# Kernel optimization log

Hardware: AMD Instinct MI355X
Metric: run time of the kernel (lower is better)

Reference implementation:

```python
import jax, jax.numpy as jnp
import numpy as np

N = 65536      # total atoms
D = 1024       # hidden_size (encoder output dim)
H = 2048       # ffn_hidden_size
OUT = 1        # output_size
M = 4096       # number of molecules (segments)


def _lin(k, fi, fo):
    return jax.random.normal(k, (fi, fo), jnp.float32) * (1.0 / np.sqrt(fi))


def setup_inputs() -> dict:
    key = jax.random.key(0)
    ks = jax.random.split(key, 14)
    hidden = jax.random.normal(ks[0], (N, D), jnp.float32)
    segment_ids = jnp.sort(jax.random.randint(ks[1], (N,), 0, M)).astype(jnp.int64)
    inp = {
        "hidden": hidden,
        "ffn_W1": _lin(ks[2], D, H), "ffn_b1": jnp.zeros((H,), jnp.float32),
        "ffn_W2": _lin(ks[3], H, H), "ffn_b2": jnp.zeros((H,), jnp.float32),
        "ffn_W3": _lin(ks[4], H, OUT), "ffn_b3": jnp.zeros((OUT,), jnp.float32),
        "wr_W1": _lin(ks[5], D, H), "wr_b1": jnp.zeros((H,), jnp.float32),
        "wr_W2": _lin(ks[6], H, H), "wr_b2": jnp.zeros((H,), jnp.float32),
        "wr_W3": _lin(ks[7], H, OUT), "wr_b3": jnp.ones((OUT,), jnp.float32),  # bias=1 keeps segment weight sums away from 0
        "segment_ids": segment_ids,
    }
    return inp


def _ffn(x, W1, b1, W2, b2, W3, b3):
    # Dropout(p) is identity in eval; activation = ReLU
    h = jax.nn.relu(x @ W1 + b1)
    h = jax.nn.relu(h @ W2 + b2)
    return h @ W3 + b3


def reference(hidden, ffn_W1, ffn_b1, ffn_W2, ffn_b2, ffn_W3, ffn_b3,
              wr_W1, wr_b1, wr_W2, wr_b2, wr_W3, wr_b3, segment_ids):
    seg = segment_ids.astype(jnp.int32)
    output = _ffn(hidden, ffn_W1, ffn_b1, ffn_W2, ffn_b2, ffn_W3, ffn_b3)   # [N, OUT]
    weights = _ffn(hidden, wr_W1, wr_b1, wr_W2, wr_b2, wr_W3, wr_b3)        # [N, OUT]
    # per-molecule sums over ALL elements of the segment slice (matches .sum())
    out_sum = jax.ops.segment_sum(output.sum(-1), seg, num_segments=M)      # [M]
    w_sum = jax.ops.segment_sum(weights.sum(-1), seg, num_segments=M)       # [M]
    ratio = (out_sum / w_sum)[seg][:, None]                                 # [N, 1]
    return output - weights * ratio
```

## Files before the change

kernel.cpp:

```cpp
#include <hip/hip_runtime.h>
#include <hip/hip_bf16.h>

#define DEVINL __device__ __forceinline__

typedef __attribute__((ext_vector_type(8))) short s8v;
typedef __attribute__((ext_vector_type(4))) float f4v;

using bf16 = __hip_bfloat16;
typedef unsigned short u16;

DEVINL u16 f2bu(float f) {
  bf16 h = __float2bfloat16(f);
  return *reinterpret_cast<u16*>(&h);
}

DEVINL void gload16(const void* g, void* l) {
  __builtin_amdgcn_global_load_lds((const __attribute__((address_space(1))) void*)g,
                                   (__attribute__((address_space(3))) void*)l, 16, 0, 0);
}

#define BAR()    __builtin_amdgcn_s_barrier()
#define LGKM(n)  asm volatile("s_waitcnt lgkmcnt(" #n ")" ::: "memory")
#define VM(n)    asm volatile("s_waitcnt vmcnt(" #n ")" ::: "memory")

__global__ void k_f32_to_bf16(const float* __restrict__ x, u16* __restrict__ y, long n4) {
  long i = (long)blockIdx.x * blockDim.x + threadIdx.x;
  if (i >= n4) return;
  float4 v = ((const float4*)x)[i];
  ushort4 o;
  o.x = f2bu(v.x); o.y = f2bu(v.y); o.z = f2bu(v.z); o.w = f2bu(v.w);
  ((ushort4*)y)[i] = o;
}

__global__ void k_transpose_bf16(const float* __restrict__ W, u16* __restrict__ Wt,
                                 int rows, int cols) {
  __shared__ float tile[32][33];
  const int tx = threadIdx.x, ty = threadIdx.y;
  const int c0 = blockIdx.x * 32, r0 = blockIdx.y * 32;
  #pragma unroll
  for (int i = ty; i < 32; i += 8)
    tile[i][tx] = W[(long)(r0 + i) * cols + (c0 + tx)];
  __syncthreads();
  #pragma unroll
  for (int i = ty; i < 32; i += 8)
    Wt[(long)(c0 + i) * rows + (r0 + tx)] = f2bu(tile[tx][i]);
}

extern __shared__ char smem[];

template<int EPI>
__global__ __launch_bounds__(512, 2)
void k_gemm8(const u16* __restrict__ A, const u16* __restrict__ Bt,
             u16* __restrict__ C, const float* __restrict__ bias,
             const float* __restrict__ w3, float* __restrict__ oacc,
             int N, int K) {
  const int tid = threadIdx.x;
  const int w = tid >> 6, lane = tid & 63;
  const int id = blockIdx.x;
  const int cpx = gridDim.x >> 3;
  const int sw = (id & 7) * cpx + (id >> 3);
  const int bn = sw & 7, bm = sw >> 3;

  const int wm = (w >> 2) * 128, wn = (w & 3) * 64;
  const int nt = K >> 6;

  f4v acc[8][4];
  #pragma unroll
  for (int i = 0; i < 8; ++i)
    #pragma unroll
    for (int jj = 0; jj < 4; ++jj)
      #pragma unroll
      for (int r = 0; r < 4; ++r) acc[i][jj][r] = 0.f;

  const int rowl = tid >> 2;
  const int jsw = (tid & 3) ^ ((rowl >> 1) & 3);
  const u16* gA = A + (long)(bm * 256 + rowl) * K + jsw * 8;
  const u16* gB = Bt + (long)(bn * 256 + rowl) * K + jsw * 8;
  const long cstr = (long)128 * K;
  const uint wb = (uint)w * 1024u;

  const uint swz = ((uint)((lane >> 4) ^ ((lane >> 1) & 3))) * 16u;
  const uint aoff = (uint)(wm + (lane & 15)) * 64u + swz;
  const uint boff = (uint)(wn + (lane & 15)) * 64u + swz + 32768u;

#define STAGE_A(pp, ks, t) do { \
    const u16* g_ = gA + (long)(t) * 64 + (ks) * 32; \
    char* l_ = smem + (uint)(pp) * 65536u + (uint)(ks) * 16384u + wb; \
    gload16(g_, l_); gload16(g_ + cstr, l_ + 8192); } while (0)
#define STAGE_B(pp, ks, t) do { \
    const u16* g_ = gB + (long)(t) * 64 + (ks) * 32; \
    char* l_ = smem + (uint)(pp) * 65536u + 32768u + (uint)(ks) * 16384u + wb; \
    gload16(g_, l_); gload16(g_ + cstr, l_ + 8192); } while (0)

#define RD_A(dst, base, ksb) do { \
    _Pragma("unroll") \
    for (int mi_ = 0; mi_ < 8; ++mi_) \
      dst[mi_] = *(const s8v*)(smem + (base) + (ksb) + aoff + (uint)mi_ * 1024u); } while (0)
#define RD_B(dst, base, ksb, c0) do { \
    dst[0] = *(const s8v*)(smem + (base) + (ksb) + boff + (uint)(c0) * 1024u); \
    dst[1] = *(const s8v*)(smem + (base) + (ksb) + boff + (uint)((c0) + 1) * 1024u); } while (0)

#define MFMA8(A_, B_, c0i, c1i) do { \
    __builtin_amdgcn_s_setprio(1); \
    _Pragma("unroll") \
    for (int mi_ = 0; mi_ < 8; ++mi_) { \
      acc[mi_][c0i] = __builtin_amdgcn_mfma_f32_16x16x32_bf16(A_[mi_], B_[0], acc[mi_][c0i], 0, 0, 0); \
      acc[mi_][c1i] = __builtin_amdgcn_mfma_f32_16x16x32_bf16(A_[mi_], B_[1], acc[mi_][c1i], 0, 0, 0); \
    } \
    __builtin_amdgcn_s_setprio(0); } while (0)

  s8v a0[8], a1[8], b01[2], b23[2];

  STAGE_A(0, 0, 0); STAGE_B(0, 0, 0); STAGE_A(0, 1, 0); STAGE_B(0, 1, 0);
  if (nt > 1) { STAGE_A(1, 0, 1); STAGE_B(1, 0, 1); VM(8); }
  else        { VM(4); }
  BAR();
  RD_A(a0, 0u, 0u); RD_B(b01, 0u, 0u, 0);

  for (int t = 0; t < nt; ++t) {
    const int p = t & 1, q = p ^ 1;
    const uint pb = (uint)p * 65536u, qb = (uint)q * 65536u;
    RD_B(b23, pb, 0u, 2);
    if (t + 1 < nt) STAGE_A(q, 1, t + 1);
    BAR(); LGKM(2);
    MFMA8(a0, b01, 0, 1);
    if (t + 1 < nt) { VM(6); } else { VM(0); }
    BAR();
    RD_A(a1, pb, 16384u); RD_B(b01, pb, 16384u, 0);
    if (t + 1 < nt) STAGE_B(q, 1, t + 1);
    LGKM(10);
    MFMA8(a0, b23, 2, 3);
    RD_B(b23, pb, 16384u, 2);
    if (t + 2 < nt) STAGE_A(p, 0, t + 2);
    BAR(); LGKM(2);
    MFMA8(a1, b01, 0, 1);
    if (t + 2 < nt) {
      STAGE_B(p, 0, t + 2);
      VM(8); BAR();
      RD_A(a0, qb, 0u); RD_B(b01, qb, 0u, 0);
      LGKM(10);
    } else if (t + 1 < nt) {
      VM(4); BAR();
      RD_A(a0, qb, 0u); RD_B(b01, qb, 0u, 0);
      LGKM(10);
    } else {
      BAR(); LGKM(0);
    }
    MFMA8(a1, b23, 2, 3);
  }

  const int crow = bm * 256 + wm + ((lane >> 4) << 2);
  const int ccol = bn * 256 + wn + (lane & 15);
  if (EPI == 1) {
    #pragma unroll
    for (int jj = 0; jj < 4; ++jj) {
      const float bb = bias[ccol + jj * 16];
      #pragma unroll
      for (int mi = 0; mi < 8; ++mi)
        #pragma unroll
        for (int r = 0; r < 4; ++r) {
          float v = acc[mi][jj][r] + bb;
          v = v > 0.f ? v : 0.f;
          C[(long)(crow + mi * 16 + r) * N + ccol + jj * 16] = f2bu(v);
        }
    }
  } else {
    float bb[4], ww[4];
    #pragma unroll
    for (int jj = 0; jj < 4; ++jj) { bb[jj] = bias[ccol + jj * 16]; ww[jj] = w3[ccol + jj * 16]; }
    #pragma unroll
    for (int mi = 0; mi < 8; ++mi)
      #pragma unroll
      for (int r = 0; r < 4; ++r) {
        float s = 0.f;
        #pragma unroll
        for (int jj = 0; jj < 4; ++jj) {
          float v = acc[mi][jj][r] + bb[jj];
          v = v > 0.f ? v : 0.f;
          s += v * ww[jj];
        }
        s += __shfl_xor(s, 1, 64);
        s += __shfl_xor(s, 2, 64);
        s += __shfl_xor(s, 4, 64);
        s += __shfl_xor(s, 8, 64);
        if ((lane & 15) == 0) atomicAdd(&oacc[crow + mi * 16 + r], s);
      }
  }
#undef STAGE_A
#undef STAGE_B
#undef RD_A
#undef RD_B
#undef MFMA8
}

__global__ void k_detect(const int* __restrict__ seg, int n, int* __restrict__ flag) {
  if (blockIdx.x == 0 && threadIdx.x == 0) flag[0] = (seg[n - 1] == 0) ? 1 : 0;
}

__global__ void k_segsum(const float* __restrict__ oacc, const float* __restrict__ wacc,
                         const int* __restrict__ seg, const int* __restrict__ flag,
                         const float* __restrict__ ob3, const float* __restrict__ wb3,
                         float* __restrict__ osum, float* __restrict__ wsum, int n) {
  int i = blockIdx.x * blockDim.x + threadIdx.x;
  if (i >= n) return;
  int s = flag[0] ? seg[2 * i] : seg[i];
  atomicAdd(&osum[s], oacc[i] + ob3[0]);
  atomicAdd(&wsum[s], wacc[i] + wb3[0]);
}

__global__ void k_final(const float* __restrict__ oacc, const float* __restrict__ wacc,
                        const int* __restrict__ seg, const int* __restrict__ flag,
                        const float* __restrict__ ob3, const float* __restrict__ wb3,
                        const float* __restrict__ osum, const float* __restrict__ wsum,
                        float* __restrict__ out, int n) {
  int i = blockIdx.x * blockDim.x + threadIdx.x;
  if (i >= n) return;
  int s = flag[0] ? seg[2 * i] : seg[i];
  float o = oacc[i] + ob3[0];
  float ww = wacc[i] + wb3[0];
  out[i] = o - ww * (osum[s] / wsum[s]);
}

extern "C" void kernel_launch(void* const* d_in, const int* in_sizes, int n_in,
                              void* d_out, int out_size, void* d_ws, size_t ws_size,
                              hipStream_t stream) {
  constexpr int NA = 65536, D = 1024, H = 2048, M = 4096;
  const float* hidden = (const float*)d_in[0];
  const float* fW1 = (const float*)d_in[1];
  const float* fb1 = (const float*)d_in[2];
  const float* fW2 = (const float*)d_in[3];
  const float* fb2 = (const float*)d_in[4];
  const float* fW3 = (const float*)d_in[5];
  const float* fb3 = (const float*)d_in[6];
  const float* wW1 = (const float*)d_in[7];
  const float* wb1 = (const float*)d_in[8];
  const float* wW2 = (const float*)d_in[9];
  const float* wb2 = (const float*)d_in[10];
  const float* wW3 = (const float*)d_in[11];
  const float* wb3 = (const float*)d_in[12];
  const int* seg = (const int*)d_in[13];
  float* out = (float*)d_out;

  char* ws = (char*)d_ws;
  size_t off = 0;
  auto alloc = [&](size_t bytes) { char* p = ws + off; off += (bytes + 255) & ~(size_t)255; return p; };
  u16* hbf  = (u16*)alloc((size_t)NA * D * 2);
  u16* w1tf = (u16*)alloc((size_t)H * D * 2);
  u16* w1tw = (u16*)alloc((size_t)H * D * 2);
  u16* w2tf = (u16*)alloc((size_t)H * H * 2);
  u16* w2tw = (u16*)alloc((size_t)H * H * 2);
  u16* h1   = (u16*)alloc((size_t)NA * H * 2);
  float* oacc = (float*)alloc((size_t)NA * 4);
  float* wacc = (float*)alloc((size_t)NA * 4);
  float* osum = (float*)alloc((size_t)M * 4);
  float* wsum = (float*)alloc((size_t)M * 4);
  int* flag = (int*)alloc(256);

  hipFuncSetAttribute((const void*)k_gemm8<1>, hipFuncAttributeMaxDynamicSharedMemorySize, 131072);
  hipFuncSetAttribute((const void*)k_gemm8<2>, hipFuncAttributeMaxDynamicSharedMemorySize, 131072);

  k_f32_to_bf16<<<(int)((long)NA * D / 4 / 256), 256, 0, stream>>>(hidden, hbf, (long)NA * D / 4);
  dim3 tb(32, 8);
  k_transpose_bf16<<<dim3(H / 32, D / 32), tb, 0, stream>>>(fW1, w1tf, D, H);
  k_transpose_bf16<<<dim3(H / 32, D / 32), tb, 0, stream>>>(wW1, w1tw, D, H);
  k_transpose_bf16<<<dim3(H / 32, H / 32), tb, 0, stream>>>(fW2, w2tf, H, H);
  k_transpose_bf16<<<dim3(H / 32, H / 32), tb, 0, stream>>>(wW2, w2tw, H, H);

  hipMemsetAsync(oacc, 0, (size_t)((char*)flag - (char*)oacc), stream);
  k_detect<<<1, 64, 0, stream>>>(seg, NA, flag);

  const int nblk = (H / 256) * (NA / 256);
  k_gemm8<1><<<nblk, 512, 131072, stream>>>(hbf, w1tf, h1, fb1, nullptr, nullptr, H, D);
  k_gemm8<2><<<nblk, 512, 131072, stream>>>(h1, w2tf, nullptr, fb2, fW3, oacc, H, H);
  k_gemm8<1><<<nblk, 512, 131072, stream>>>(hbf, w1tw, h1, wb1, nullptr, nullptr, H, D);
  k_gemm8<2><<<nblk, 512, 131072, stream>>>(h1, w2tw, nullptr, wb2, wW3, wacc, H, H);

  k_segsum<<<NA / 256, 256, 0, stream>>>(oacc, wacc, seg, flag, fb3, wb3, osum, wsum, NA);
  k_final<<<NA / 256, 256, 0, stream>>>(oacc, wacc, seg, flag, fb3, wb3, osum, wsum, out, NA);
}
```

Baseline: 1.936 ms.

## Simplify GEMM main loop to single A register set with full waits

```diff
diff --git a/kernel.cpp b/kernel.cpp
--- a/kernel.cpp
+++ b/kernel.cpp
@@ -20,8 +20,9 @@
 }
 
 #define BAR()    __builtin_amdgcn_s_barrier()
-#define LGKM(n)  asm volatile("s_waitcnt lgkmcnt(" #n ")" ::: "memory")
+#define LGKM0()  asm volatile("s_waitcnt lgkmcnt(0)" ::: "memory")
 #define VM(n)    asm volatile("s_waitcnt vmcnt(" #n ")" ::: "memory")
+#define SCHED0() __builtin_amdgcn_sched_barrier(0)
 
 __global__ void k_f32_to_bf16(const float* __restrict__ x, u16* __restrict__ y, long n4) {
   long i = (long)blockIdx.x * blockDim.x + threadIdx.x;
@@ -109,44 +110,39 @@
     } \
     __builtin_amdgcn_s_setprio(0); } while (0)
 
-  s8v a0[8], a1[8], b01[2], b23[2];
+  s8v a[8], b01[2], b23[2];
 
   STAGE_A(0, 0, 0); STAGE_B(0, 0, 0); STAGE_A(0, 1, 0); STAGE_B(0, 1, 0);
   if (nt > 1) { STAGE_A(1, 0, 1); STAGE_B(1, 0, 1); VM(8); }
   else        { VM(4); }
   BAR();
-  RD_A(a0, 0u, 0u); RD_B(b01, 0u, 0u, 0);
 
   for (int t = 0; t < nt; ++t) {
     const int p = t & 1, q = p ^ 1;
-    const uint pb = (uint)p * 65536u, qb = (uint)q * 65536u;
+    const uint pb = (uint)p * 65536u;
+    RD_A(a, pb, 0u); RD_B(b01, pb, 0u, 0);
+    if (t + 1 < nt) STAGE_A(q, 1, t + 1);
+    BAR(); LGKM0(); SCHED0();
+    MFMA8(a, b01, 0, 1);
+    BAR();
     RD_B(b23, pb, 0u, 2);
-    if (t + 1 < nt) STAGE_A(q, 1, t + 1);
-    BAR(); LGKM(2);
-    MFMA8(a0, b01, 0, 1);
-    if (t + 1 < nt) { VM(6); } else { VM(0); }
-    BAR();
-    RD_A(a1, pb, 16384u); RD_B(b01, pb, 16384u, 0);
-    if (t + 1 < nt) STAGE_B(q, 1, t + 1);
-    LGKM(10);
-    MFMA8(a0, b23, 2, 3);
+    if (t + 1 < nt) { STAGE_B(q, 1, t + 1); VM(8); }
+    else            { VM(0); }
+    BAR(); LGKM0(); SCHED0();
+    MFMA8(a, b23, 2, 3);
+    BAR();
+    RD_A(a, pb, 16384u); RD_B(b01, pb, 16384u, 0);
+    if (t + 2 < nt) STAGE_A(p, 0, t + 2);
+    BAR(); LGKM0(); SCHED0();
+    MFMA8(a, b01, 0, 1);
+    BAR();
     RD_B(b23, pb, 16384u, 2);
-    if (t + 2 < nt) STAGE_A(p, 0, t + 2);
-    BAR(); LGKM(2);
-    MFMA8(a1, b01, 0, 1);
-    if (t + 2 < nt) {
-      STAGE_B(p, 0, t + 2);
-      VM(8); BAR();
-      RD_A(a0, qb, 0u); RD_B(b01, qb, 0u, 0);
-      LGKM(10);
-    } else if (t + 1 < nt) {
-      VM(4); BAR();
-      RD_A(a0, qb, 0u); RD_B(b01, qb, 0u, 0);
-      LGKM(10);
-    } else {
-      BAR(); LGKM(0);
-    }
-    MFMA8(a1, b23, 2, 3);
+    if (t + 2 < nt)      { STAGE_B(p, 0, t + 2); VM(8); }
+    else if (t + 1 < nt) { VM(4); }
+    else                 { VM(0); }
+    BAR(); LGKM0(); SCHED0();
+    MFMA8(a, b23, 2, 3);
+    BAR();
   }
 
   const int crow = bm * 256 + wm + ((lane >> 4) << 2);
```

Result: slower. 1.975 ms (+2.0%).
